# Optimization experiments

Hardware: AMD Instinct MI355X
Metric: run time of the kernel (lower is better)

The kernel has to match this reference:

```python
import jax, jax.numpy as jnp
import numpy as np

B, H = 16384, 1024
EPS = 1e-5


def setup_inputs() -> dict:
    key = jax.random.key(0)
    ks = jax.random.split(key, 12)
    inp = {
        "t": 0,
        "h": jax.random.normal(ks[0], (B, H), jnp.float32),
        "e": jax.random.normal(ks[1], (B, H), jnp.float32),
        # LiquidNeuron params
        "W_rec": jax.random.normal(ks[2], (H, H), jnp.float32) * 0.1,
        "bias": jnp.zeros((H,), jnp.float32),
        "tau": jnp.ones((H,), jnp.float32),
        "decay": jnp.ones((H,), jnp.float32),
        "ln_w": jnp.ones((H,), jnp.float32),
        "ln_b": jnp.zeros((H,), jnp.float32),
        # context_encoder: Linear -> ReLU -> Linear (dropout = identity in eval)
        "ce_w1": jax.random.normal(ks[3], (H, H), jnp.float32) * (1.0 / np.sqrt(H)),
        "ce_b1": jnp.zeros((H,), jnp.float32),
        "ce_w2": jax.random.normal(ks[4], (H, H), jnp.float32) * (1.0 / np.sqrt(H)),
        "ce_b2": jnp.zeros((H,), jnp.float32),
        # param_modulator
        "pm_w": jax.random.normal(ks[5], (H, H), jnp.float32) * (1.0 / np.sqrt(H)),
        "pm_b": jnp.zeros((H,), jnp.float32),
    }
    return inp


def reference(t, h, e, W_rec, bias, tau, decay, ln_w, ln_b,
              ce_w1, ce_b1, ce_w2, ce_b2, pm_w, pm_b):
    # context encoder (eval mode: dropout is identity)
    context = jnp.maximum(h @ ce_w1.T + ce_b1, 0.0) @ ce_w2.T + ce_b2  # [B,H]
    pa = context @ pm_w.T + pm_b  # param_adjustment [B,H]
    # bmm(e[:,None,:], (W_rec*(1+pa)[:,:,None]).T) == (1+pa) * (e @ W_rec.T)
    matmul_result = (1.0 + pa) * (e @ W_rec.T)  # [B,H]
    tau_adjusted = tau * jax.nn.sigmoid(pa)  # [B,H]
    dh_dt = (-decay * h + matmul_result + bias) / tau_adjusted
    # LayerNorm over last dim
    mu = jnp.mean(dh_dt, axis=-1, keepdims=True)
    var = jnp.var(dh_dt, axis=-1, keepdims=True)
    dh_dt = (dh_dt - mu) * jax.lax.rsqrt(var + EPS) * ln_w + ln_b
    return dh_dt
```

## Files before the change

kernel.cpp:

```cpp
#include <hip/hip_runtime.h>
#include <stdint.h>

#define H_DIM 1024
#define B_DIM 16384

typedef unsigned short u16;
typedef short bf16x8 __attribute__((ext_vector_type(8)));
typedef unsigned short ushort8 __attribute__((ext_vector_type(8)));
typedef float f32x4 __attribute__((ext_vector_type(4)));

__device__ __forceinline__ u16 f2bf(float f) {
  union { float f; uint32_t u; } v; v.f = f;
  uint32_t r = v.u + 0x7fffu + ((v.u >> 16) & 1u);
  return (u16)(r >> 16);
}
__device__ __forceinline__ float bf2f(u16 x) {
  union { uint32_t u; float f; } v; v.u = ((uint32_t)x) << 16;
  return v.f;
}

#define GLDS16(gsrc, ldst)                                                                 \
  __builtin_amdgcn_global_load_lds((const __attribute__((address_space(1))) void*)(gsrc),  \
                                   (__attribute__((address_space(3))) void*)(ldst), 16, 0, 0)

__global__ __launch_bounds__(256) void cvt2_f32_bf16(const float* __restrict__ a0,
                                                     const float* __restrict__ a1,
                                                     u16* __restrict__ o0,
                                                     u16* __restrict__ o1) {
  const int which = blockIdx.x >> 11;
  const float* in = which ? a1 : a0;
  u16* out = which ? o1 : o0;
  const int n4 = (B_DIM * H_DIM) / 4;
  int i = (blockIdx.x & 2047) * 256 + threadIdx.x;
  const float4* in4 = (const float4*)in;
  ushort4* out4 = (ushort4*)out;
  for (; i < n4; i += 2048 * 256) {
    float4 v = in4[i];
    ushort4 o;
    o.x = f2bf(v.x); o.y = f2bf(v.y); o.z = f2bf(v.z); o.w = f2bf(v.w);
    out4[i] = o;
  }
}

__global__ __launch_bounds__(256) void cvt4_f32_bf16(const float* __restrict__ a0,
                                                     const float* __restrict__ a1,
                                                     const float* __restrict__ a2,
                                                     const float* __restrict__ a3,
                                                     u16* __restrict__ o0, u16* __restrict__ o1,
                                                     u16* __restrict__ o2, u16* __restrict__ o3,
                                                     const float* __restrict__ tau,
                                                     float* __restrict__ rtau) {
  if (blockIdx.x >= 1024) {
    for (int i = threadIdx.x; i < H_DIM; i += 256) rtau[i] = 1.0f / tau[i];
    return;
  }
  const int which = blockIdx.x >> 8;
  const float* in = which == 0 ? a0 : which == 1 ? a1 : which == 2 ? a2 : a3;
  u16* out = which == 0 ? o0 : which == 1 ? o1 : which == 2 ? o2 : o3;
  const int n4 = (H_DIM * H_DIM) / 4;
  int i = (blockIdx.x & 255) * 256 + threadIdx.x;
  const float4* in4 = (const float4*)in;
  ushort4* out4 = (ushort4*)out;
  for (; i < n4; i += 256 * 256) {
    float4 v = in4[i];
    ushort4 o;
    o.x = f2bf(v.x); o.y = f2bf(v.y); o.z = f2bf(v.z); o.w = f2bf(v.w);
    out4[i] = o;
  }
}


template <int MODE>
__device__ __forceinline__ void subtile_step(u16* shp, int slot, int slot3, int aoff, int boff,
                                             int wv, const u16*& pA0, const u16*& pA1,
                                             const u16*& pB0, const u16*& pB1,
                                             f32x4 (&acc)[8][4]) {
  const u16* Ab = shp + slot * 16384 + aoff;
  const u16* Bb = shp + slot * 16384 + 8192 + boff;
  bf16x8 aF[8], bF[4];
#pragma unroll
  for (int i = 0; i < 4; ++i) aF[i] = *(const bf16x8*)(Ab + i * 512);
#pragma unroll
  for (int i = 0; i < 4; ++i) bF[i] = *(const bf16x8*)(Bb + i * 512);
#pragma unroll
  for (int i = 4; i < 8; ++i) aF[i] = *(const bf16x8*)(Ab + i * 512);
  if (MODE == 3) {
    u16* da = shp + slot3 * 16384 + wv * 1024;
    GLDS16(pA0, da); GLDS16(pA1, da + 512);
    u16* db = shp + slot3 * 16384 + 8192 + wv * 1024;
    GLDS16(pB0, db); GLDS16(pB1, db + 512);
    pA0 += 32; pA1 += 32; pB0 += 32; pB1 += 32;
  }
  __builtin_amdgcn_s_setprio(1);
#pragma unroll
  for (int mf = 0; mf < 4; ++mf)
#pragma unroll
    for (int nf = 0; nf < 4; ++nf)
      acc[mf][nf] = __builtin_amdgcn_mfma_f32_16x16x32_bf16(aF[mf], bF[nf], acc[mf][nf], 0, 0, 0);
#pragma unroll
  for (int mf = 4; mf < 8; ++mf)
#pragma unroll
    for (int nf = 0; nf < 4; ++nf)
      acc[mf][nf] = __builtin_amdgcn_mfma_f32_16x16x32_bf16(aF[mf], bF[nf], acc[mf][nf], 0, 0, 0);
  __builtin_amdgcn_s_setprio(0);
  if (MODE == 3) asm volatile("s_waitcnt vmcnt(8)" ::: "memory");
  if (MODE == 2) asm volatile("s_waitcnt vmcnt(4)" ::: "memory");
  if (MODE == 1) asm volatile("s_waitcnt vmcnt(0)" ::: "memory");
  __builtin_amdgcn_s_barrier();
}

template <bool RELU, bool HASBIAS, typename OUT>
__global__ __launch_bounds__(512, 2) void gemm256(const u16* __restrict__ A,
                                                  const u16* __restrict__ W,
                                                  const float* __restrict__ bias,
                                                  OUT* __restrict__ C) {
  extern __shared__ u16 sh[];
  const int t = threadIdx.x;
  const int wv = t >> 6, l = t & 63;
  const int wm = wv >> 2, wn = wv & 3;
  const int l15 = l & 15, lg = l >> 4;

  const int bid = blockIdx.x;
  const int logical = (bid & 7) * 32 + (bid >> 3);
  const int m0 = (logical >> 2) * 256;
  const int n0 = (logical & 3) * 256;

  const int koff = (lg ^ ((l15 >> 1) & 3)) * 8;
  const int aoff = (wm * 128 + l15) * 32 + koff;
  const int boff = (wn * 64 + l15) * 32 + koff;

  const int rowst = wv * 32 + (l >> 2);
  const int ksl = ((l & 3) ^ ((l >> 3) & 3)) * 8;
  const u16* pA0 = A + (size_t)(m0 + rowst) * H_DIM + ksl;
  const u16* pA1 = pA0 + 16 * H_DIM;
  const u16* pB0 = W + (size_t)(n0 + rowst) * H_DIM + ksl;
  const u16* pB1 = pB0 + 16 * H_DIM;

  f32x4 acc[8][4] = {};

#pragma unroll
  for (int s = 0; s < 3; ++s) {
    u16* da = sh + s * 16384 + wv * 1024;
    GLDS16(pA0, da); GLDS16(pA1, da + 512);
    u16* db = sh + s * 16384 + 8192 + wv * 1024;
    GLDS16(pB0, db); GLDS16(pB1, db + 512);
    pA0 += 32; pA1 += 32; pB0 += 32; pB1 += 32;
  }
  asm volatile("s_waitcnt vmcnt(8)" ::: "memory");
  __builtin_amdgcn_s_barrier();

  for (int s = 0; s < 29; ++s)
    subtile_step<3>(sh, s & 3, (s + 3) & 3, aoff, boff, wv, pA0, pA1, pB0, pB1, acc);
  subtile_step<2>(sh, 1, 0, aoff, boff, wv, pA0, pA1, pB0, pB1, acc);
  subtile_step<1>(sh, 2, 0, aoff, boff, wv, pA0, pA1, pB0, pB1, acc);
  subtile_step<0>(sh, 3, 0, aoff, boff, wv, pA0, pA1, pB0, pB1, acc);

  float bv[4];
#pragma unroll
  for (int nf = 0; nf < 4; ++nf)
    bv[nf] = HASBIAS ? bias[n0 + wn * 64 + nf * 16 + l15] : 0.0f;
#pragma unroll
  for (int mf = 0; mf < 8; ++mf) {
#pragma unroll
    for (int nf = 0; nf < 4; ++nf) {
      const int col = n0 + wn * 64 + nf * 16 + l15;
#pragma unroll
      for (int j = 0; j < 4; ++j) {
        const int row = m0 + wm * 128 + mf * 16 + lg * 4 + j;
        float v = acc[mf][nf][j] + bv[nf];
        if (RELU) v = fmaxf(v, 0.0f);
        if constexpr (sizeof(OUT) == 2)
          C[(size_t)row * H_DIM + col] = (OUT)f2bf(v);
        else
          C[(size_t)row * H_DIM + col] = v;
      }
    }
  }
}

__global__ __launch_bounds__(256) void liquid_ln(const float* __restrict__ h,
                                                 const u16* __restrict__ pa,
                                                 const u16* __restrict__ ev,
                                                 const float* __restrict__ bias,
                                                 const float* __restrict__ rtau,
                                                 const float* __restrict__ decay,
                                                 const float* __restrict__ lnw,
                                                 const float* __restrict__ lnb,
                                                 float* __restrict__ out) {
  const int wv = threadIdx.x >> 6, l = threadIdx.x & 63;
  const int row = blockIdx.x * 4 + wv;
  const size_t rb = (size_t)row * H_DIM;

  float d[16];
  float s = 0.f, ss = 0.f;
#pragma unroll
  for (int c = 0; c < 2; ++c) {
    const int col = c * 512 + l * 8;
    float h8[8], b8[8], r8[8], dc8[8];
    *(float4*)h8 = *(const float4*)(h + rb + col);
    *(float4*)(h8 + 4) = *(const float4*)(h + rb + col + 4);
    *(float4*)b8 = *(const float4*)(bias + col);
    *(float4*)(b8 + 4) = *(const float4*)(bias + col + 4);
    *(float4*)r8 = *(const float4*)(rtau + col);
    *(float4*)(r8 + 4) = *(const float4*)(rtau + col + 4);
    *(float4*)dc8 = *(const float4*)(decay + col);
    *(float4*)(dc8 + 4) = *(const float4*)(decay + col + 4);
    ushort8 pv = *(const ushort8*)(pa + rb + col);
    ushort8 evv = *(const ushort8*)(ev + rb + col);
#pragma unroll
    for (int j = 0; j < 8; ++j) {
      const float p = bf2f(pv[j]);
      const float e = bf2f(evv[j]);
      const float num = fmaf(-dc8[j], h8[j], fmaf(1.0f + p, e, b8[j]));
      const float val = num * (1.0f + __expf(-p)) * r8[j];
      d[c * 8 + j] = val;
      s += val;
      ss += val * val;
    }
  }
#pragma unroll
  for (int off = 32; off; off >>= 1) {
    s += __shfl_xor(s, off);
    ss += __shfl_xor(ss, off);
  }
  const float mu = s * (1.0f / H_DIM);
  const float var = ss * (1.0f / H_DIM) - mu * mu;
  const float rstd = rsqrtf(var + 1e-5f);

#pragma unroll
  for (int c = 0; c < 2; ++c) {
    const int col = c * 512 + l * 8;
    float w8[8], lb8[8], o[8];
    *(float4*)w8 = *(const float4*)(lnw + col);
    *(float4*)(w8 + 4) = *(const float4*)(lnw + col + 4);
    *(float4*)lb8 = *(const float4*)(lnb + col);
    *(float4*)(lb8 + 4) = *(const float4*)(lnb + col + 4);
#pragma unroll
    for (int j = 0; j < 8; ++j) o[j] = fmaf((d[c * 8 + j] - mu) * rstd, w8[j], lb8[j]);
    *(float4*)(out + rb + col) = *(float4*)o;
    *(float4*)(out + rb + col + 4) = *(float4*)(o + 4);
  }
}

extern "C" void kernel_launch(void* const* d_in, const int* in_sizes, int n_in,
                              void* d_out, int out_size, void* d_ws, size_t ws_size,
                              hipStream_t stream) {
  const float* h = (const float*)d_in[1];
  const float* e = (const float*)d_in[2];
  const float* Wrec = (const float*)d_in[3];
  const float* bias = (const float*)d_in[4];
  const float* tau = (const float*)d_in[5];
  const float* decay = (const float*)d_in[6];
  const float* lnw = (const float*)d_in[7];
  const float* lnb = (const float*)d_in[8];
  const float* ce_w1 = (const float*)d_in[9];
  const float* ce_b1 = (const float*)d_in[10];
  const float* ce_w2 = (const float*)d_in[11];
  const float* ce_b2 = (const float*)d_in[12];
  const float* pm_w = (const float*)d_in[13];
  const float* pm_b = (const float*)d_in[14];
  float* out = (float*)d_out;

  char* ws = (char*)d_ws;
  const size_t MB = 1024 * 1024;
  u16* w1b = (u16*)(ws + 0 * MB);
  u16* w2b = (u16*)(ws + 2 * MB);
  u16* w3b = (u16*)(ws + 4 * MB);
  u16* w4b = (u16*)(ws + 6 * MB);
  u16* ebf = (u16*)(ws + 8 * MB);
  u16* hbf = (u16*)(ws + 40 * MB);
  u16* t1 = (u16*)(ws + 72 * MB);
  u16* ctx = (u16*)(ws + 104 * MB);
  u16* pab = (u16*)(ws + 40 * MB);
  u16* evb = (u16*)(ws + 104 * MB);
  float* rtau = (float*)(ws + 150 * MB);

  cvt2_f32_bf16<<<4096, 256, 0, stream>>>(h, e, hbf, ebf);
  cvt4_f32_bf16<<<1025, 256, 0, stream>>>(ce_w1, ce_w2, pm_w, Wrec, w1b, w2b, w3b, w4b, tau, rtau);

  const int LDS_BYTES = 131072;
  hipFuncSetAttribute((const void*)gemm256<true, true, u16>,
                      hipFuncAttributeMaxDynamicSharedMemorySize, LDS_BYTES);
  hipFuncSetAttribute((const void*)gemm256<false, true, u16>,
                      hipFuncAttributeMaxDynamicSharedMemorySize, LDS_BYTES);
  hipFuncSetAttribute((const void*)gemm256<false, false, u16>,
                      hipFuncAttributeMaxDynamicSharedMemorySize, LDS_BYTES);

  const int NWG = (B_DIM / 256) * (H_DIM / 256);
  gemm256<true, true, u16><<<NWG, 512, LDS_BYTES, stream>>>(hbf, w1b, ce_b1, t1);
  gemm256<false, true, u16><<<NWG, 512, LDS_BYTES, stream>>>(t1, w2b, ce_b2, ctx);
  gemm256<false, true, u16><<<NWG, 512, LDS_BYTES, stream>>>(ctx, w3b, pm_b, pab);
  gemm256<false, false, u16><<<NWG, 512, LDS_BYTES, stream>>>(ebf, w4b, nullptr, evb);

  liquid_ln<<<B_DIM / 4, 256, 0, stream>>>(h, pab, evb, bias, rtau, decay, lnw, lnb, out);
}
```

Baseline: 220.4 us.

## Fuse fp32-to-bf16 activation conversion into GEMM A-operand loading

Drops the separate kernel that converted h and e to bf16. A new GEMM variant reads fp32 A tiles into registers, converts them to bf16 and writes them to LDS, with a register prefetch several stages deep, while B still uses direct global-to-LDS loads. This avoids writing and re-reading 64MB of bf16 activations and one kernel launch. In exchange, A global traffic doubles inside the GEMM (fp32 instead of bf16) and register pressure rises, which could hurt MFMA overlap.

```diff
diff --git a/kernel.cpp b/kernel.cpp
--- a/kernel.cpp
+++ b/kernel.cpp
@@ -22,25 +22,6 @@
 #define GLDS16(gsrc, ldst)                                                                 \
   __builtin_amdgcn_global_load_lds((const __attribute__((address_space(1))) void*)(gsrc),  \
                                    (__attribute__((address_space(3))) void*)(ldst), 16, 0, 0)
-
-__global__ __launch_bounds__(256) void cvt2_f32_bf16(const float* __restrict__ a0,
-                                                     const float* __restrict__ a1,
-                                                     u16* __restrict__ o0,
-                                                     u16* __restrict__ o1) {
-  const int which = blockIdx.x >> 11;
-  const float* in = which ? a1 : a0;
-  u16* out = which ? o1 : o0;
-  const int n4 = (B_DIM * H_DIM) / 4;
-  int i = (blockIdx.x & 2047) * 256 + threadIdx.x;
-  const float4* in4 = (const float4*)in;
-  ushort4* out4 = (ushort4*)out;
-  for (; i < n4; i += 2048 * 256) {
-    float4 v = in4[i];
-    ushort4 o;
-    o.x = f2bf(v.x); o.y = f2bf(v.y); o.z = f2bf(v.z); o.w = f2bf(v.w);
-    out4[i] = o;
-  }
-}
 
 __global__ __launch_bounds__(256) void cvt4_f32_bf16(const float* __restrict__ a0,
                                                      const float* __restrict__ a1,
@@ -69,7 +50,6 @@
   }
 }
 
-
 template <int MODE>
 __device__ __forceinline__ void subtile_step(u16* shp, int slot, int slot3, int aoff, int boff,
                                              int wv, const u16*& pA0, const u16*& pA1,
@@ -173,6 +153,168 @@
           C[(size_t)row * H_DIM + col] = (OUT)f2bf(v);
         else
           C[(size_t)row * H_DIM + col] = v;
+      }
+    }
+  }
+}
+
+template <int P, bool DO_A, bool DO_B, bool DO_W, int VE>
+__device__ __forceinline__ void step_f32a(u16* sh, int aoff, int boff, int wv, int l,
+                                          const float*& gA, const u16*& pB0, const u16*& pB1,
+                                          f32x4 (&ra)[4][4], f32x4 (&acc)[8][4]) {
+  constexpr int WSLOT = (P + 2) & 3;
+  constexpr int BSLOT = (P + 3) & 3;
+  const u16* Ab = sh + P * 16384 + aoff;
+  const u16* Bb = sh + P * 16384 + 8192 + boff;
+  bf16x8 aF[8], bF[4];
+#pragma unroll
+  for (int i = 0; i < 4; ++i) aF[i] = *(const bf16x8*)(Ab + i * 512);
+#pragma unroll
+  for (int i = 0; i < 4; ++i) bF[i] = *(const bf16x8*)(Bb + i * 512);
+#pragma unroll
+  for (int i = 4; i < 8; ++i) aF[i] = *(const bf16x8*)(Ab + i * 512);
+  if constexpr (DO_W) {
+    ushort8 w0, w1;
+#pragma unroll
+    for (int j = 0; j < 4; ++j) {
+      w0[j] = f2bf(ra[P][0][j]);
+      w0[4 + j] = f2bf(ra[P][1][j]);
+      w1[j] = f2bf(ra[P][2][j]);
+      w1[4 + j] = f2bf(ra[P][3][j]);
+    }
+    u16* dw = sh + WSLOT * 16384 + wv * 1024 + l * 8;
+    *(ushort8*)dw = w0;
+    *(ushort8*)(dw + 512) = w1;
+  }
+  if constexpr (DO_A) {
+    ra[WSLOT][0] = *(const f32x4*)(gA);
+    ra[WSLOT][1] = *(const f32x4*)(gA + 4);
+    ra[WSLOT][2] = *(const f32x4*)(gA + 16 * H_DIM);
+    ra[WSLOT][3] = *(const f32x4*)(gA + 16 * H_DIM + 4);
+    gA += 32;
+  }
+  if constexpr (DO_B) {
+    u16* db = sh + BSLOT * 16384 + 8192 + wv * 1024;
+    GLDS16(pB0, db);
+    GLDS16(pB1, db + 512);
+    pB0 += 32;
+    pB1 += 32;
+  }
+  __builtin_amdgcn_s_setprio(1);
+#pragma unroll
+  for (int mf = 0; mf < 4; ++mf)
+#pragma unroll
+    for (int nf = 0; nf < 4; ++nf)
+      acc[mf][nf] = __builtin_amdgcn_mfma_f32_16x16x32_bf16(aF[mf], bF[nf], acc[mf][nf], 0, 0, 0);
+#pragma unroll
+  for (int mf = 4; mf < 8; ++mf)
+#pragma unroll
+    for (int nf = 0; nf < 4; ++nf)
+      acc[mf][nf] = __builtin_amdgcn_mfma_f32_16x16x32_bf16(aF[mf], bF[nf], acc[mf][nf], 0, 0, 0);
+  __builtin_amdgcn_s_setprio(0);
+  if constexpr (VE == 12) asm volatile("s_waitcnt vmcnt(12)" ::: "memory");
+  if constexpr (VE == 8) asm volatile("s_waitcnt vmcnt(8)" ::: "memory");
+  if constexpr (VE == 2) asm volatile("s_waitcnt vmcnt(2)" ::: "memory");
+  if constexpr (VE == 0) asm volatile("s_waitcnt vmcnt(0)" ::: "memory");
+  asm volatile("s_waitcnt lgkmcnt(0)" ::: "memory");
+  __builtin_amdgcn_s_barrier();
+}
+
+template <bool RELU, bool HASBIAS>
+__global__ __launch_bounds__(512, 1) void gemm256_f32a(const float* __restrict__ A,
+                                                       const u16* __restrict__ W,
+                                                       const float* __restrict__ bias,
+                                                       u16* __restrict__ C) {
+  extern __shared__ u16 sh[];
+  const int t = threadIdx.x;
+  const int wv = t >> 6, l = t & 63;
+  const int wm = wv >> 2, wn = wv & 3;
+  const int l15 = l & 15, lg = l >> 4;
+
+  const int bid = blockIdx.x;
+  const int logical = (bid & 7) * 32 + (bid >> 3);
+  const int m0 = (logical >> 2) * 256;
+  const int n0 = (logical & 3) * 256;
+
+  const int koff = (lg ^ ((l15 >> 1) & 3)) * 8;
+  const int aoff = (wm * 128 + l15) * 32 + koff;
+  const int boff = (wn * 64 + l15) * 32 + koff;
+
+  const int rowst = wv * 32 + (l >> 2);
+  const int ksl = ((l & 3) ^ ((l >> 3) & 3)) * 8;
+  const float* gA = A + (size_t)(m0 + rowst) * H_DIM + ksl;
+  const u16* pB0 = W + (size_t)(n0 + rowst) * H_DIM + ksl;
+  const u16* pB1 = pB0 + 16 * H_DIM;
+
+  f32x4 acc[8][4] = {};
+  f32x4 ra[4][4];
+
+  f32x4 t0[4], t1v[4];
+  t0[0] = *(const f32x4*)(gA); t0[1] = *(const f32x4*)(gA + 4);
+  t0[2] = *(const f32x4*)(gA + 16 * H_DIM); t0[3] = *(const f32x4*)(gA + 16 * H_DIM + 4);
+  gA += 32;
+  t1v[0] = *(const f32x4*)(gA); t1v[1] = *(const f32x4*)(gA + 4);
+  t1v[2] = *(const f32x4*)(gA + 16 * H_DIM); t1v[3] = *(const f32x4*)(gA + 16 * H_DIM + 4);
+  gA += 32;
+  ra[0][0] = *(const f32x4*)(gA); ra[0][1] = *(const f32x4*)(gA + 4);
+  ra[0][2] = *(const f32x4*)(gA + 16 * H_DIM); ra[0][3] = *(const f32x4*)(gA + 16 * H_DIM + 4);
+  gA += 32;
+  ra[1][0] = *(const f32x4*)(gA); ra[1][1] = *(const f32x4*)(gA + 4);
+  ra[1][2] = *(const f32x4*)(gA + 16 * H_DIM); ra[1][3] = *(const f32x4*)(gA + 16 * H_DIM + 4);
+  gA += 32;
+#pragma unroll
+  for (int s = 0; s < 3; ++s) {
+    u16* db = sh + s * 16384 + 8192 + wv * 1024;
+    GLDS16(pB0, db); GLDS16(pB1, db + 512);
+    pB0 += 32; pB1 += 32;
+  }
+  {
+    ushort8 w0, w1;
+#pragma unroll
+    for (int j = 0; j < 4; ++j) {
+      w0[j] = f2bf(t0[0][j]); w0[4 + j] = f2bf(t0[1][j]);
+      w1[j] = f2bf(t0[2][j]); w1[4 + j] = f2bf(t0[3][j]);
+    }
+    u16* dw = sh + wv * 1024 + l * 8;
+    *(ushort8*)dw = w0; *(ushort8*)(dw + 512) = w1;
+#pragma unroll
+    for (int j = 0; j < 4; ++j) {
+      w0[j] = f2bf(t1v[0][j]); w0[4 + j] = f2bf(t1v[1][j]);
+      w1[j] = f2bf(t1v[2][j]); w1[4 + j] = f2bf(t1v[3][j]);
+    }
+    dw = sh + 16384 + wv * 1024 + l * 8;
+    *(ushort8*)dw = w0; *(ushort8*)(dw + 512) = w1;
+  }
+  asm volatile("s_waitcnt vmcnt(0)" ::: "memory");
+  asm volatile("s_waitcnt lgkmcnt(0)" ::: "memory");
+  __builtin_amdgcn_s_barrier();
+
+  for (int su = 0; su < 7; ++su) {
+    step_f32a<0, true, true, true, 12>(sh, aoff, boff, wv, l, gA, pB0, pB1, ra, acc);
+    step_f32a<1, true, true, true, 12>(sh, aoff, boff, wv, l, gA, pB0, pB1, ra, acc);
+    step_f32a<2, true, true, true, 12>(sh, aoff, boff, wv, l, gA, pB0, pB1, ra, acc);
+    step_f32a<3, true, true, true, 12>(sh, aoff, boff, wv, l, gA, pB0, pB1, ra, acc);
+  }
+  step_f32a<0, false, true, true, 8>(sh, aoff, boff, wv, l, gA, pB0, pB1, ra, acc);
+  step_f32a<1, false, false, true, 2>(sh, aoff, boff, wv, l, gA, pB0, pB1, ra, acc);
+  step_f32a<2, false, false, false, 0>(sh, aoff, boff, wv, l, gA, pB0, pB1, ra, acc);
+  step_f32a<3, false, false, false, -1>(sh, aoff, boff, wv, l, gA, pB0, pB1, ra, acc);
+
+  float bv[4];
+#pragma unroll
+  for (int nf = 0; nf < 4; ++nf)
+    bv[nf] = HASBIAS ? bias[n0 + wn * 64 + nf * 16 + l15] : 0.0f;
+#pragma unroll
+  for (int mf = 0; mf < 8; ++mf) {
+#pragma unroll
+    for (int nf = 0; nf < 4; ++nf) {
+      const int col = n0 + wn * 64 + nf * 16 + l15;
+#pragma unroll
+      for (int j = 0; j < 4; ++j) {
+        const int row = m0 + wm * 128 + mf * 16 + lg * 4 + j;
+        float v = acc[mf][nf][j] + bv[nf];
+        if (RELU) v = fmaxf(v, 0.0f);
+        C[(size_t)row * H_DIM + col] = f2bf(v);
       }
     }
   }
@@ -267,30 +409,27 @@
   u16* w2b = (u16*)(ws + 2 * MB);
   u16* w3b = (u16*)(ws + 4 * MB);
   u16* w4b = (u16*)(ws + 6 * MB);
-  u16* ebf = (u16*)(ws + 8 * MB);
-  u16* hbf = (u16*)(ws + 40 * MB);
-  u16* t1 = (u16*)(ws + 72 * MB);
-  u16* ctx = (u16*)(ws + 104 * MB);
-  u16* pab = (u16*)(ws + 40 * MB);
+  u16* t1 = (u16*)(ws + 8 * MB);
+  u16* ctx = (u16*)(ws + 40 * MB);
+  u16* pab = (u16*)(ws + 72 * MB);
   u16* evb = (u16*)(ws + 104 * MB);
-  float* rtau = (float*)(ws + 150 * MB);
-
-  cvt2_f32_bf16<<<4096, 256, 0, stream>>>(h, e, hbf, ebf);
+  float* rtau = (float*)(ws + 136 * MB);
+
   cvt4_f32_bf16<<<1025, 256, 0, stream>>>(ce_w1, ce_w2, pm_w, Wrec, w1b, w2b, w3b, w4b, tau, rtau);
 
   const int LDS_BYTES = 131072;
-  hipFuncSetAttribute((const void*)gemm256<true, true, u16>,
+  hipFuncSetAttribute((const void*)gemm256_f32a<true, true>,
+                      hipFuncAttributeMaxDynamicSharedMemorySize, LDS_BYTES);
+  hipFuncSetAttribute((const void*)gemm256_f32a<false, false>,
                       hipFuncAttributeMaxDynamicSharedMemorySize, LDS_BYTES);
   hipFuncSetAttribute((const void*)gemm256<false, true, u16>,
                       hipFuncAttributeMaxDynamicSharedMemorySize, LDS_BYTES);
-  hipFuncSetAttribute((const void*)gemm256<false, false, u16>,
-                      hipFuncAttributeMaxDynamicSharedMemorySize, LDS_BYTES);
 
   const int NWG = (B_DIM / 256) * (H_DIM / 256);
-  gemm256<true, true, u16><<<NWG, 512, LDS_BYTES, stream>>>(hbf, w1b, ce_b1, t1);
+  gemm256_f32a<true, true><<<NWG, 512, LDS_BYTES, stream>>>(h, w1b, ce_b1, t1);
   gemm256<false, true, u16><<<NWG, 512, LDS_BYTES, stream>>>(t1, w2b, ce_b2, ctx);
   gemm256<false, true, u16><<<NWG, 512, LDS_BYTES, stream>>>(ctx, w3b, pm_b, pab);
-  gemm256<false, false, u16><<<NWG, 512, LDS_BYTES, stream>>>(ebf, w4b, nullptr, evb);
+  gemm256_f32a<false, false><<<NWG, 512, LDS_BYTES, stream>>>(e, w4b, nullptr, evb);
 
   liquid_ln<<<B_DIM / 4, 256, 0, stream>>>(h, pab, evb, bias, rtau, decay, lnw, lnb, out);
 }
```

Measured after the change: 282.3 us. 28.1% more time.
